# Performance work log

Measured on AMD Instinct MI355X. Metric: run time of the kernel, lower is better.

Reference implementation:

```python
import jax, jax.numpy as jnp
import numpy as np
from jax import lax

B, S, F, D, O = 4096, 256, 32, 64, 16
LABEL = S // 2  # label site index (num_sites // 2)


def setup_inputs() -> dict:
    key = jax.random.key(0)
    k = jax.random.split(key, 6)
    x = jax.random.normal(k[0], (B, S, F), dtype=jnp.float32)
    # Variance-preserving scales so the 256-step chain stays O(1)
    s_edge = 1.0 / np.sqrt(F)
    s_mid = 1.0 / np.sqrt(D * F)
    s_lab = 1.0 / np.sqrt(D * F * D)
    W0 = jax.random.normal(k[1], (F, D), dtype=jnp.float32) * s_edge          # site 0
    W_left = jax.random.normal(k[2], (LABEL - 1, D, F, D), dtype=jnp.float32) * s_mid   # sites 1..LABEL-1
    W_label = jax.random.normal(k[3], (D, F, D, O), dtype=jnp.float32) * s_lab          # site LABEL
    W_right = jax.random.normal(k[4], (S - 2 - LABEL, D, F, D), dtype=jnp.float32) * s_mid  # sites LABEL+1..S-2 (ascending)
    W_last = jax.random.normal(k[5], (D, F), dtype=jnp.float32) * s_edge       # site S-1
    return {"x": x, "W0": W0, "W_left": W_left, "W_label": W_label,
            "W_right": W_right, "W_last": W_last}


def _mps_forward(x, W0, W_left, W_label, W_right, W_last):
    label = W_left.shape[0] + 1
    # left sweep: v_b = x[b,0] @ W0, then v <- v W(x_i)
    v = jnp.einsum('bf,fd->bd', x[:, 0], W0)                 # (B, D)
    xs_left = jnp.moveaxis(x[:, 1:label], 0, 1)              # (L_left, B, F)

    def lstep(v, inp):
        W, xi = inp                                          # (D,F,D), (B,F)
        return jnp.einsum('bd,dfe,bf->be', v, W, xi), None

    v, _ = lax.scan(lstep, v, (W_left, xs_left))

    # right sweep: r_b = W_last @ x[b,-1], then r <- W(x_i) r, i from S-2 down to label+1
    r = jnp.einsum('bf,df->bd', x[:, -1], W_last)            # (B, D)
    xs_right = jnp.moveaxis(x[:, label + 1:-1], 0, 1)        # (L_right, B, F)

    def rstep(r, inp):
        W, xi = inp
        return jnp.einsum('be,dfe,bf->bd', r, W, xi), None

    r, _ = lax.scan(rstep, r, (W_right, xs_right), reverse=True)

    # label site contraction -> logits (B, O)
    return jnp.einsum('bd,dfeo,bf,be->bo', v, W_label, x[:, label], r)


def reference(x, W0, W_left, W_label, W_right, W_last):
    return _mps_forward(x, W0, W_left, W_label, W_right, W_last)
```

## Files before the change

### kernel.cpp

```cpp
#include <hip/hip_runtime.h>


typedef _Float16 half2v __attribute__((ext_vector_type(2)));
typedef _Float16 half8 __attribute__((ext_vector_type(8)));
typedef float f32x16 __attribute__((ext_vector_type(16)));
typedef unsigned int uint4v __attribute__((ext_vector_type(4)));

#define MFMA32(a, b, c) __builtin_amdgcn_mfma_f32_32x32x16_f16((a), (b), (c), 0, 0, 0)

#define VPAD 66

#define WS_WLF 0L
#define WS_WRF 33292288L
#define WS_WLAB 66322432L
#define WS_V 70516736L
#define WS_R 71565312L

__device__ __forceinline__ f32x16 zero16() {
  f32x16 z;
#pragma unroll
  for (int i = 0; i < 16; ++i) z[i] = 0.0f;
  return z;
}

__device__ __forceinline__ unsigned int pack2h(float a, float b) {
  half2v h;
  h[0] = (_Float16)a;
  h[1] = (_Float16)b;
  return __builtin_bit_cast(unsigned int, h);
}

__device__ __forceinline__ half2v splat2(float a) {
  _Float16 x = (_Float16)a;
  half2v h;
  h[0] = x;
  h[1] = x;
  return h;
}

__device__ __forceinline__ half8 mulfrag(const half2v s, const unsigned int* o) {
  uint4v t;
#pragma unroll
  for (int i = 0; i < 4; ++i) {
    half2v b = __builtin_bit_cast(half2v, o[i]);
    half2v p = s * b;
    t[i] = __builtin_bit_cast(unsigned int, p);
  }
  return __builtin_bit_cast(half8, t);
}

__global__ void prep_kernel(const float* __restrict__ wl, const float* __restrict__ wr,
                            const float* __restrict__ wlab,
                            _Float16* __restrict__ wlf, _Float16* __restrict__ wrf,
                            _Float16* __restrict__ wlabf) {
  const long t0 = (long)blockIdx.x * blockDim.x + threadIdx.x;
  const long stride = (long)gridDim.x * blockDim.x;
  const long NL = 127L * 128 * 2 * 64;
  const long NR = 126L * 128 * 2 * 64;
  const long NB = 128L * 32 * 64;

  for (long F = t0; F < NL; F += stride) {
    const int l = (int)(F & 63), t = (int)((F >> 6) & 1);
    const int s = (int)((F >> 7) & 127), site = (int)(F >> 14);
    const int k0 = s * 16 + ((l >> 5) << 3);
    const int d = k0 >> 5, f0 = k0 & 31, e = t * 32 + (l & 31);
    const float* src = wl + (((long)site * 64 + d) * 32 + f0) * 64 + e;
    half8 v;
#pragma unroll
    for (int j = 0; j < 8; ++j) v[j] = (_Float16)src[(long)j * 64];
    *(half8*)(wlf + F * 8) = v;
  }
  for (long F = t0; F < NR; F += stride) {
    const int l = (int)(F & 63), t = (int)((F >> 6) & 1);
    const int s = (int)((F >> 7) & 127), site = (int)(F >> 14);
    const int k0 = s * 16 + ((l >> 5) << 3);
    const int f = k0 >> 6, e0 = k0 & 63, d = t * 32 + (l & 31);
    const float* src = wr + (((long)site * 64 + d) * 32 + f) * 64 + e0;
    half8 v;
#pragma unroll
    for (int j = 0; j < 8; ++j) v[j] = (_Float16)src[j];
    *(half8*)(wrf + F * 8) = v;
  }
  for (long F = t0; F < NB; F += stride) {
    const int l = (int)(F & 63), t = (int)((F >> 6) & 31);
    const int s = (int)(F >> 11);
    const int k0 = s * 16 + ((l >> 5) << 3);
    const int d = k0 >> 5, f0 = k0 & 31;
    const int n = t * 32 + (l & 31);
    const int e = n >> 4, oo = n & 15;
    const float* src = wlab + (((long)d * 32 + f0) * 64 + e) * 16 + oo;
    half8 v;
#pragma unroll
    for (int j = 0; j < 8; ++j) v[j] = (_Float16)src[(long)j * 1024];
    *(half8*)(wlabf + F * 8) = v;
  }
}

__launch_bounds__(1024, 4)
__global__ void chain_kernel(const float* __restrict__ x, const float* __restrict__ w0,
                             const float* __restrict__ wlast,
                             const _Float16* __restrict__ wlf,
                             const _Float16* __restrict__ wrf,
                             float* __restrict__ wsV, float* __restrict__ wsR) {
  __shared__ float vacc[2][32 * VPAD];
  __shared__ unsigned int xsf[2][2][64][4];
  __shared__ unsigned int xplu[2][32][17];
  __shared__ float xinit[32][33];

  const int tid = threadIdx.x;
  const int lane = tid & 63;
  const int wv = tid >> 6;
  const int t = wv & 1;
  const int kq = wv >> 1;
  const int m = lane & 31;
  const int h = lane >> 5;
  const int chain = blockIdx.x >> 7;
  const int b0 = (blockIdx.x & 127) * 32;

  if (tid < 128) {
    const int row = tid >> 2, c8 = (tid & 3) * 8;
    const float* xp = x + ((long)(b0 + row) * 256 + (chain ? 255 : 0)) * 32 + c8;
    const float4 xa = ((const float4*)xp)[0];
    const float4 xb = ((const float4*)xp)[1];
    xinit[row][c8 + 0] = xa.x; xinit[row][c8 + 1] = xa.y;
    xinit[row][c8 + 2] = xa.z; xinit[row][c8 + 3] = xa.w;
    xinit[row][c8 + 4] = xb.x; xinit[row][c8 + 5] = xb.y;
    xinit[row][c8 + 6] = xb.z; xinit[row][c8 + 7] = xb.w;
  }
  __syncthreads();
  {
    const int row = tid >> 5, c = tid & 31;
    float a0 = 0.f, a1 = 0.f;
    if (chain == 0) {
#pragma unroll 8
      for (int f = 0; f < 32; ++f) {
        a0 += xinit[row][f] * w0[f * 64 + c];
        a1 += xinit[row][f] * w0[f * 64 + c + 32];
      }
    } else {
#pragma unroll 8
      for (int f = 0; f < 32; ++f) {
        a0 += xinit[row][f] * wlast[c * 32 + f];
        a1 += xinit[row][f] * wlast[(c + 32) * 32 + f];
      }
    }
    vacc[1][row * VPAD + c] = a0;
    vacc[1][row * VPAD + c + 32] = a1;
  }
  if (tid < 512) {
    const int row = tid >> 4, q = tid & 15;
    const float2 f2 = *(const float2*)(x + ((long)(b0 + row) * 256 + (chain ? 254 : 1)) * 32 + 2 * q);
    const unsigned int pk = pack2h(f2.x, f2.y);
    if (chain == 0)
      xsf[0][q >> 3][((q >> 2) & 1) * 32 + row][q & 3] = pk;
    else
      xplu[0][row][q] = pk;
  }
  __syncthreads();

  const int NIT = chain ? 126 : 127;

  for (int it = 0; it < NIT; ++it) {
    float* P = vacc[it & 1];
    const float* Q = vacc[(it + 1) & 1];
    const int cb = it & 1, nb = (it & 1) ^ 1;

    for (int i = tid; i < 32 * VPAD; i += 1024) P[i] = 0.f;

    half2v vsp[8];
    unsigned int roct[4][4];
    if (chain == 0) {
      const float* src = Q + m * VPAD + kq * 8;
#pragma unroll
      for (int qq = 0; qq < 4; ++qq) {
        const float2 f2 = *(const float2*)(src + 2 * qq);
        vsp[2 * qq] = splat2(f2.x);
        vsp[2 * qq + 1] = splat2(f2.y);
      }
    } else {
      const float* src = Q + m * VPAD + 8 * h;
#pragma unroll
      for (int c = 0; c < 4; ++c)
#pragma unroll
        for (int i = 0; i < 4; ++i) {
          const float2 f2 = *(const float2*)(src + 16 * c + 2 * i);
          roct[c][i] = pack2h(f2.x, f2.y);
        }
    }
    __syncthreads();

    float2 pxf;
    const bool haspx = (it + 1 < NIT) && (tid < 512);
    if (haspx) {
      const int row = tid >> 4, q = tid & 15;
      const int nsite = chain ? (253 - it) : (2 + it);
      pxf = *(const float2*)(x + ((long)(b0 + row) * 256 + nsite) * 32 + 2 * q);
    }

    f32x16 acc = zero16();

    if (chain == 0) {
      unsigned int xo[2][4];
#pragma unroll
      for (int p = 0; p < 2; ++p)
#pragma unroll
        for (int i = 0; i < 4; ++i) xo[p][i] = xsf[cb][p][lane][i];

      const _Float16* wb = wlf + (long)it * 131072 + kq * 16384 + t * 512 + lane * 8;
#pragma unroll
      for (int q = 0; q < 8; ++q) {
        half8 bp0 = *(const half8*)(wb + q * 2048);
        half8 bp1 = *(const half8*)(wb + q * 2048 + 1024);
        half8 a0 = mulfrag(vsp[q], xo[0]);
        half8 a1 = mulfrag(vsp[q], xo[1]);
        acc = MFMA32(a0, bp0, acc);
        acc = MFMA32(a1, bp1, acc);
      }
    } else {
      const _Float16* wb = wrf + (long)(125 - it) * 131072 + kq * 16384 + t * 512 + lane * 8;
#pragma unroll
      for (int q = 0; q < 4; ++q) {
        const int fi = 4 * kq + q;
        const half2v pw = __builtin_bit_cast(half2v, xplu[cb][m][fi >> 1]);
        const _Float16 xv = (fi & 1) ? pw[1] : pw[0];
        half2v sp;
        sp[0] = xv;
        sp[1] = xv;
#pragma unroll
        for (int c = 0; c < 4; ++c) {
          half8 b = *(const half8*)(wb + q * 4096 + c * 1024);
          half8 a = mulfrag(sp, roct[c]);
          acc = MFMA32(a, b, acc);
        }
      }
    }

    if (haspx) {
      const int row = tid >> 4, q = tid & 15;
      const unsigned int pk = pack2h(pxf.x, pxf.y);
      if (chain == 0)
        xsf[nb][q >> 3][((q >> 2) & 1) * 32 + row][q & 3] = pk;
      else
        xplu[nb][row][q] = pk;
    }

#pragma unroll
    for (int gg = 0; gg < 16; ++gg) {
      const int g = (gg + 2 * kq) & 15;
      const int r = (g & 3) + ((g >> 2) << 3) + (h << 2);
      atomicAdd(&P[r * VPAD + t * 32 + m], acc[g]);
    }
    __syncthreads();
  }

  {
    const float* FB = vacc[(NIT - 1) & 1];
    float* dst = (chain ? wsR : wsV) + (long)b0 * 64;
    for (int i = tid; i < 2048; i += 1024) dst[i] = FB[(i >> 6) * VPAD + (i & 63)];
  }
}

__launch_bounds__(1024, 4)
__global__ void label_kernel(const float* __restrict__ x,
                             const _Float16* __restrict__ wlabf,
                             const float* __restrict__ wsV, const float* __restrict__ wsR,
                             float* __restrict__ out) {
  __shared__ float vsh[32 * VPAD];
  __shared__ float rsh[32 * VPAD];
  __shared__ unsigned int xsf[2][64][4];
  __shared__ float lacc[32][17];

  const int tid = threadIdx.x, lane = tid & 63, wv = tid >> 6;
  const int t = wv & 1, kq = wv >> 1;
  const int m = lane & 31, h = lane >> 5;
  const long b0 = (long)blockIdx.x * 32;

  for (int i = tid; i < 2048; i += 1024) {
    vsh[(i >> 6) * VPAD + (i & 63)] = wsV[b0 * 64 + i];
    rsh[(i >> 6) * VPAD + (i & 63)] = wsR[b0 * 64 + i];
  }
  if (tid < 544) ((float*)lacc)[tid] = 0.f;
  if (tid < 512) {
    const int row = tid >> 4, q = tid & 15;
    const float2 f2 = *(const float2*)(x + ((b0 + row) * 256 + 128) * 32 + 2 * q);
    xsf[q >> 3][((q >> 2) & 1) * 32 + row][q & 3] = pack2h(f2.x, f2.y);
  }
  __syncthreads();

  half2v vsp[8];
  {
    const float* src = vsh + m * VPAD + kq * 8;
#pragma unroll
    for (int qq = 0; qq < 4; ++qq) {
      const float2 f2 = *(const float2*)(src + 2 * qq);
      vsp[2 * qq] = splat2(f2.x);
      vsp[2 * qq + 1] = splat2(f2.y);
    }
  }
  unsigned int xo[2][4];
#pragma unroll
  for (int p = 0; p < 2; ++p)
#pragma unroll
    for (int i = 0; i < 4; ++i) xo[p][i] = xsf[p][lane][i];

  float lg[16];
#pragma unroll
  for (int g = 0; g < 16; ++g) lg[g] = 0.f;

  const _Float16* wb = wlabf + (long)kq * 16 * 16384 + t * 512 + lane * 8;
  for (int g2 = 0; g2 < 16; ++g2) {
    f32x16 acc = zero16();
    const _Float16* wg = wb + (long)g2 * 1024;
#pragma unroll
    for (int q = 0; q < 8; ++q) {
      half8 bp0 = *(const half8*)(wg + (long)q * 32768);
      half8 bp1 = *(const half8*)(wg + (long)q * 32768 + 16384);
      half8 a0 = mulfrag(vsp[q], xo[0]);
      half8 a1 = mulfrag(vsp[q], xo[1]);
      acc = MFMA32(a0, bp0, acc);
      acc = MFMA32(a1, bp1, acc);
    }
    const int e = g2 * 4 + t * 2 + (m >> 4);
#pragma unroll
    for (int g = 0; g < 16; ++g) {
      const int r = (g & 3) + ((g >> 2) << 3) + (h << 2);
      lg[g] += acc[g] * rsh[r * VPAD + e];
    }
  }
#pragma unroll
  for (int gg = 0; gg < 16; ++gg) {
    const int g = (gg + 2 * kq) & 15;
    const int r = (g & 3) + ((g >> 2) << 3) + (h << 2);
    atomicAdd(&lacc[r][m & 15], lg[g]);
  }
  __syncthreads();
  if (tid < 512) out[b0 * 16 + tid] = lacc[tid >> 4][tid & 15];
}

extern "C" void kernel_launch(void* const* d_in, const int* in_sizes, int n_in,
                              void* d_out, int out_size, void* d_ws, size_t ws_size,
                              hipStream_t stream) {
  const float* x = (const float*)d_in[0];
  const float* w0 = (const float*)d_in[1];
  const float* wl = (const float*)d_in[2];
  const float* wlab = (const float*)d_in[3];
  const float* wr = (const float*)d_in[4];
  const float* wlast = (const float*)d_in[5];

  char* ws = (char*)d_ws;
  _Float16* wlf = (_Float16*)(ws + WS_WLF);
  _Float16* wrf = (_Float16*)(ws + WS_WRF);
  _Float16* wlabf = (_Float16*)(ws + WS_WLAB);
  float* wsV = (float*)(ws + WS_V);
  float* wsR = (float*)(ws + WS_R);

  prep_kernel<<<2048, 256, 0, stream>>>(wl, wr, wlab, wlf, wrf, wlabf);
  chain_kernel<<<256, 1024, 0, stream>>>(x, w0, wlast, wlf, wrf, wsV, wsR);
  label_kernel<<<128, 1024, 0, stream>>>(x, wlabf, wsV, wsR, (float*)d_out);
}
```

Baseline: 3.598 ms.

## Prefetch weight fragments before barrier and use lgkm-only barriers in chain loop

In the chain kernel, all 16 weight fragments for the step are loaded from global memory into registers at the top of each iteration, before the shared-memory zeroing and the barrier. Their latency can then overlap with the barrier and the LDS reads. __syncthreads is replaced by an s_waitcnt lgkmcnt(0) plus s_barrier, so the barrier does not also wait on outstanding global loads. The x-operand LDS reads are moved ahead of the barrier. The label kernel also batches its weight loads into two groups of eight. This raises register pressure under 1024-thread launch bounds, and the hand-written barrier relies on the global prefetch staying outside the LDS dependency.

```diff
diff --git a/kernel.cpp b/kernel.cpp
--- a/kernel.cpp
+++ b/kernel.cpp
@@ -15,6 +15,12 @@
 #define WS_WLAB 66322432L
 #define WS_V 70516736L
 #define WS_R 71565312L
+
+#define LGKM_BARRIER()                                   \
+  do {                                                   \
+    asm volatile("s_waitcnt lgkmcnt(0)" ::: "memory");   \
+    __builtin_amdgcn_s_barrier();                        \
+  } while (0)
 
 __device__ __forceinline__ f32x16 zero16() {
   f32x16 z;
@@ -165,29 +171,14 @@
     const float* Q = vacc[(it + 1) & 1];
     const int cb = it & 1, nb = (it & 1) ^ 1;
 
-    for (int i = tid; i < 32 * VPAD; i += 1024) P[i] = 0.f;
-
-    half2v vsp[8];
-    unsigned int roct[4][4];
-    if (chain == 0) {
-      const float* src = Q + m * VPAD + kq * 8;
-#pragma unroll
-      for (int qq = 0; qq < 4; ++qq) {
-        const float2 f2 = *(const float2*)(src + 2 * qq);
-        vsp[2 * qq] = splat2(f2.x);
-        vsp[2 * qq + 1] = splat2(f2.y);
-      }
-    } else {
-      const float* src = Q + m * VPAD + 8 * h;
-#pragma unroll
-      for (int c = 0; c < 4; ++c)
-#pragma unroll
-        for (int i = 0; i < 4; ++i) {
-          const float2 f2 = *(const float2*)(src + 16 * c + 2 * i);
-          roct[c][i] = pack2h(f2.x, f2.y);
-        }
-    }
-    __syncthreads();
+    half8 wbuf[16];
+    {
+      const _Float16* wb = (chain == 0)
+          ? (wlf + (long)it * 131072 + kq * 16384 + t * 512 + lane * 8)
+          : (wrf + (long)(125 - it) * 131072 + kq * 16384 + t * 512 + lane * 8);
+#pragma unroll
+      for (int i = 0; i < 16; ++i) wbuf[i] = *(const half8*)(wb + i * 1024);
+    }
 
     float2 pxf;
     const bool haspx = (it + 1 < NIT) && (tid < 512);
@@ -197,40 +188,59 @@
       pxf = *(const float2*)(x + ((long)(b0 + row) * 256 + nsite) * 32 + 2 * q);
     }
 
+    for (int i = tid; i < 32 * VPAD; i += 1024) P[i] = 0.f;
+
+    half2v vsp[8];
+    unsigned int roct[4][4];
+    unsigned int xo[2][4];
+    unsigned int xw0 = 0, xw1 = 0;
+    if (chain == 0) {
+      const float* src = Q + m * VPAD + kq * 8;
+#pragma unroll
+      for (int qq = 0; qq < 4; ++qq) {
+        const float2 f2 = *(const float2*)(src + 2 * qq);
+        vsp[2 * qq] = splat2(f2.x);
+        vsp[2 * qq + 1] = splat2(f2.y);
+      }
+#pragma unroll
+      for (int p = 0; p < 2; ++p)
+#pragma unroll
+        for (int i = 0; i < 4; ++i) xo[p][i] = xsf[cb][p][lane][i];
+    } else {
+      const float* src = Q + m * VPAD + 8 * h;
+#pragma unroll
+      for (int c = 0; c < 4; ++c)
+#pragma unroll
+        for (int i = 0; i < 4; ++i) {
+          const float2 f2 = *(const float2*)(src + 16 * c + 2 * i);
+          roct[c][i] = pack2h(f2.x, f2.y);
+        }
+      xw0 = xplu[cb][m][2 * kq];
+      xw1 = xplu[cb][m][2 * kq + 1];
+    }
+    LGKM_BARRIER();
+
     f32x16 acc = zero16();
-
     if (chain == 0) {
-      unsigned int xo[2][4];
-#pragma unroll
-      for (int p = 0; p < 2; ++p)
-#pragma unroll
-        for (int i = 0; i < 4; ++i) xo[p][i] = xsf[cb][p][lane][i];
-
-      const _Float16* wb = wlf + (long)it * 131072 + kq * 16384 + t * 512 + lane * 8;
 #pragma unroll
       for (int q = 0; q < 8; ++q) {
-        half8 bp0 = *(const half8*)(wb + q * 2048);
-        half8 bp1 = *(const half8*)(wb + q * 2048 + 1024);
         half8 a0 = mulfrag(vsp[q], xo[0]);
+        acc = MFMA32(a0, wbuf[2 * q], acc);
         half8 a1 = mulfrag(vsp[q], xo[1]);
-        acc = MFMA32(a0, bp0, acc);
-        acc = MFMA32(a1, bp1, acc);
+        acc = MFMA32(a1, wbuf[2 * q + 1], acc);
       }
     } else {
-      const _Float16* wb = wrf + (long)(125 - it) * 131072 + kq * 16384 + t * 512 + lane * 8;
 #pragma unroll
       for (int q = 0; q < 4; ++q) {
-        const int fi = 4 * kq + q;
-        const half2v pw = __builtin_bit_cast(half2v, xplu[cb][m][fi >> 1]);
-        const _Float16 xv = (fi & 1) ? pw[1] : pw[0];
+        const half2v pw = __builtin_bit_cast(half2v, (q & 2) ? xw1 : xw0);
+        const _Float16 xv = (q & 1) ? pw[1] : pw[0];
         half2v sp;
         sp[0] = xv;
         sp[1] = xv;
 #pragma unroll
         for (int c = 0; c < 4; ++c) {
-          half8 b = *(const half8*)(wb + q * 4096 + c * 1024);
           half8 a = mulfrag(sp, roct[c]);
-          acc = MFMA32(a, b, acc);
+          acc = MFMA32(a, wbuf[4 * q + c], acc);
         }
       }
     }
@@ -250,7 +260,7 @@
       const int r = (g & 3) + ((g >> 2) << 3) + (h << 2);
       atomicAdd(&P[r * VPAD + t * 32 + m], acc[g]);
     }
-    __syncthreads();
+    LGKM_BARRIER();
   }
 
   {
@@ -311,14 +321,24 @@
   for (int g2 = 0; g2 < 16; ++g2) {
     f32x16 acc = zero16();
     const _Float16* wg = wb + (long)g2 * 1024;
-#pragma unroll
-    for (int q = 0; q < 8; ++q) {
-      half8 bp0 = *(const half8*)(wg + (long)q * 32768);
-      half8 bp1 = *(const half8*)(wg + (long)q * 32768 + 16384);
+    half8 wbuf[8];
+#pragma unroll
+    for (int i = 0; i < 8; ++i) wbuf[i] = *(const half8*)(wg + (long)i * 16384);
+#pragma unroll
+    for (int q = 0; q < 4; ++q) {
       half8 a0 = mulfrag(vsp[q], xo[0]);
+      acc = MFMA32(a0, wbuf[2 * q], acc);
       half8 a1 = mulfrag(vsp[q], xo[1]);
-      acc = MFMA32(a0, bp0, acc);
-      acc = MFMA32(a1, bp1, acc);
+      acc = MFMA32(a1, wbuf[2 * q + 1], acc);
+    }
+#pragma unroll
+    for (int i = 0; i < 8; ++i) wbuf[i] = *(const half8*)(wg + (long)(8 + i) * 16384);
+#pragma unroll
+    for (int q = 4; q < 8; ++q) {
+      half8 a0 = mulfrag(vsp[q], xo[0]);
+      acc = MFMA32(a0, wbuf[2 * (q - 4)], acc);
+      half8 a1 = mulfrag(vsp[q], xo[1]);
+      acc = MFMA32(a1, wbuf[2 * (q - 4) + 1], acc);
     }
     const int e = g2 * 4 + t * 2 + (m >> 4);
 #pragma unroll
```

New measurement: 4.203 ms. 16.8% more time.

## Stream chain weights through LDS ring buffer with async global-to-LDS loads

Applied to the files above, without the earlier changes.

The chain kernel now stages each 32KB weight phase into a 4-slot LDS ring buffer via global_load_lds, issued three phases ahead, with manual vmcnt/barrier waits. The reduction split changes so each wave handles one phase slice from LDS instead of loading directly from global. The label kernel batches its weight loads into register groups of eight before the MFMAs. The aim is to hide global-memory latency in the sequential chain. In exchange it adds 128KB of LDS and a barrier per phase, which lowers occupancy and adds synchronisation.

```diff
diff --git a/kernel.cpp b/kernel.cpp
--- a/kernel.cpp
+++ b/kernel.cpp
@@ -47,6 +47,12 @@
     t[i] = __builtin_bit_cast(unsigned int, p);
   }
   return __builtin_bit_cast(half8, t);
+}
+
+__device__ __forceinline__ void gll16(const _Float16* g, _Float16* l) {
+  __builtin_amdgcn_global_load_lds(
+      (const __attribute__((address_space(1))) void*)g,
+      (__attribute__((address_space(3))) void*)l, 16, 0, 0);
 }
 
 __global__ void prep_kernel(const float* __restrict__ wl, const float* __restrict__ wr,
@@ -102,30 +108,43 @@
                              const _Float16* __restrict__ wlf,
                              const _Float16* __restrict__ wrf,
                              float* __restrict__ wsV, float* __restrict__ wsR) {
+  __shared__ __align__(16) _Float16 wstage[4][16384];
   __shared__ float vacc[2][32 * VPAD];
   __shared__ unsigned int xsf[2][2][64][4];
   __shared__ unsigned int xplu[2][32][17];
-  __shared__ float xinit[32][33];
 
   const int tid = threadIdx.x;
   const int lane = tid & 63;
   const int wv = tid >> 6;
   const int t = wv & 1;
-  const int kq = wv >> 1;
+  const int ks = wv >> 1;
   const int m = lane & 31;
   const int h = lane >> 5;
   const int chain = blockIdx.x >> 7;
   const int b0 = (blockIdx.x & 127) * 32;
-
+  const int NIT = chain ? 126 : 127;
+  const int gmax = NIT * 8 - 1;
+
+  auto stage = [&](int g) {
+    const int gc = (g <= gmax) ? g : gmax;
+    const int st = gc >> 3, ph = gc & 7;
+    const _Float16* base = chain ? (wrf + (long)(125 - st) * 131072)
+                                 : (wlf + (long)st * 131072);
+    const _Float16* gsrc = base + (long)ph * 16384 + (2 * wv) * 512 + lane * 8;
+    _Float16* ldst = &wstage[gc & 3][(2 * wv) * 512];
+    gll16(gsrc, ldst);
+    gll16(gsrc + 512, ldst + 512);
+  };
+
+  float* xinit = (float*)&wstage[0][0];
   if (tid < 128) {
     const int row = tid >> 2, c8 = (tid & 3) * 8;
     const float* xp = x + ((long)(b0 + row) * 256 + (chain ? 255 : 0)) * 32 + c8;
     const float4 xa = ((const float4*)xp)[0];
     const float4 xb = ((const float4*)xp)[1];
-    xinit[row][c8 + 0] = xa.x; xinit[row][c8 + 1] = xa.y;
-    xinit[row][c8 + 2] = xa.z; xinit[row][c8 + 3] = xa.w;
-    xinit[row][c8 + 4] = xb.x; xinit[row][c8 + 5] = xb.y;
-    xinit[row][c8 + 6] = xb.z; xinit[row][c8 + 7] = xb.w;
+    float* d = xinit + row * 33 + c8;
+    d[0] = xa.x; d[1] = xa.y; d[2] = xa.z; d[3] = xa.w;
+    d[4] = xb.x; d[5] = xb.y; d[6] = xb.z; d[7] = xb.w;
   }
   __syncthreads();
   {
@@ -134,14 +153,14 @@
     if (chain == 0) {
 #pragma unroll 8
       for (int f = 0; f < 32; ++f) {
-        a0 += xinit[row][f] * w0[f * 64 + c];
-        a1 += xinit[row][f] * w0[f * 64 + c + 32];
+        a0 += xinit[row * 33 + f] * w0[f * 64 + c];
+        a1 += xinit[row * 33 + f] * w0[f * 64 + c + 32];
       }
     } else {
 #pragma unroll 8
       for (int f = 0; f < 32; ++f) {
-        a0 += xinit[row][f] * wlast[c * 32 + f];
-        a1 += xinit[row][f] * wlast[(c + 32) * 32 + f];
+        a0 += xinit[row * 33 + f] * wlast[c * 32 + f];
+        a1 += xinit[row * 33 + f] * wlast[(c + 32) * 32 + f];
       }
     }
     vacc[1][row * VPAD + c] = a0;
@@ -158,36 +177,15 @@
   }
   __syncthreads();
 
-  const int NIT = chain ? 126 : 127;
+  stage(0);
+  stage(1);
+  stage(2);
 
   for (int it = 0; it < NIT; ++it) {
     float* P = vacc[it & 1];
     const float* Q = vacc[(it + 1) & 1];
-    const int cb = it & 1, nb = (it & 1) ^ 1;
-
-    for (int i = tid; i < 32 * VPAD; i += 1024) P[i] = 0.f;
-
-    half2v vsp[8];
-    unsigned int roct[4][4];
-    if (chain == 0) {
-      const float* src = Q + m * VPAD + kq * 8;
-#pragma unroll
-      for (int qq = 0; qq < 4; ++qq) {
-        const float2 f2 = *(const float2*)(src + 2 * qq);
-        vsp[2 * qq] = splat2(f2.x);
-        vsp[2 * qq + 1] = splat2(f2.y);
-      }
-    } else {
-      const float* src = Q + m * VPAD + 8 * h;
-#pragma unroll
-      for (int c = 0; c < 4; ++c)
-#pragma unroll
-        for (int i = 0; i < 4; ++i) {
-          const float2 f2 = *(const float2*)(src + 16 * c + 2 * i);
-          roct[c][i] = pack2h(f2.x, f2.y);
-        }
-    }
-    __syncthreads();
+    const int cb = it & 1, nb = cb ^ 1;
+    const int it8 = it * 8;
 
     float2 pxf;
     const bool haspx = (it + 1 < NIT) && (tid < 512);
@@ -197,43 +195,62 @@
       pxf = *(const float2*)(x + ((long)(b0 + row) * 256 + nsite) * 32 + 2 * q);
     }
 
-    f32x16 acc = zero16();
-
+    for (int i = tid; i < 32 * VPAD; i += 1024) P[i] = 0.f;
+
+    half2v spl[8];
+    unsigned int oct2[2][4];
     if (chain == 0) {
-      unsigned int xo[2][4];
-#pragma unroll
-      for (int p = 0; p < 2; ++p)
-#pragma unroll
-        for (int i = 0; i < 4; ++i) xo[p][i] = xsf[cb][p][lane][i];
-
-      const _Float16* wb = wlf + (long)it * 131072 + kq * 16384 + t * 512 + lane * 8;
-#pragma unroll
-      for (int q = 0; q < 8; ++q) {
-        half8 bp0 = *(const half8*)(wb + q * 2048);
-        half8 bp1 = *(const half8*)(wb + q * 2048 + 1024);
-        half8 a0 = mulfrag(vsp[q], xo[0]);
-        half8 a1 = mulfrag(vsp[q], xo[1]);
-        acc = MFMA32(a0, bp0, acc);
-        acc = MFMA32(a1, bp1, acc);
+#pragma unroll
+      for (int p = 0; p < 8; ++p) spl[p] = splat2(Q[m * VPAD + 8 * p + ks]);
+#pragma unroll
+      for (int i = 0; i < 4; ++i) {
+        oct2[0][i] = xsf[cb][0][lane][i];
+        oct2[1][i] = xsf[cb][1][lane][i];
       }
     } else {
-      const _Float16* wb = wrf + (long)(125 - it) * 131072 + kq * 16384 + t * 512 + lane * 8;
-#pragma unroll
-      for (int q = 0; q < 4; ++q) {
-        const int fi = 4 * kq + q;
-        const half2v pw = __builtin_bit_cast(half2v, xplu[cb][m][fi >> 1]);
-        const _Float16 xv = (fi & 1) ? pw[1] : pw[0];
-        half2v sp;
-        sp[0] = xv;
-        sp[1] = xv;
-#pragma unroll
-        for (int c = 0; c < 4; ++c) {
-          half8 b = *(const half8*)(wb + q * 4096 + c * 1024);
-          half8 a = mulfrag(sp, roct[c]);
-          acc = MFMA32(a, b, acc);
+      const int kh = ks >> 1;
+#pragma unroll
+      for (int p = 0; p < 8; ++p) {
+        const half2v pw = __builtin_bit_cast(half2v, xplu[cb][m][2 * p + (kh >> 1)]);
+        const _Float16 xv = (kh & 1) ? pw[1] : pw[0];
+        half2v sp; sp[0] = xv; sp[1] = xv;
+        spl[p] = sp;
+      }
+      const int e0 = (ks & 1) * 32 + 8 * h;
+#pragma unroll
+      for (int c = 0; c < 2; ++c)
+#pragma unroll
+        for (int i = 0; i < 4; ++i) {
+          const float2 f2 = *(const float2*)(Q + m * VPAD + e0 + 16 * c + 2 * i);
+          oct2[c][i] = pack2h(f2.x, f2.y);
         }
-      }
-    }
+    }
+    asm volatile("s_waitcnt lgkmcnt(0)" ::: "memory");
+    __builtin_amdgcn_s_barrier();
+    asm volatile("" ::: "memory");
+
+    f32x16 acc = zero16();
+
+#define PHASE(p)                                                               \
+    {                                                                          \
+      asm volatile("s_waitcnt vmcnt(4) lgkmcnt(0)" ::: "memory");              \
+      __builtin_amdgcn_s_barrier();                                            \
+      asm volatile("" ::: "memory");                                           \
+      stage(it8 + (p) + 3);                                                    \
+      {                                                                        \
+        const _Float16* W =                                                    \
+            &wstage[(p) & 3][0] + (4 * ks + t) * 512 + lane * 8;               \
+        const half8 bA = *(const half8*)(W);                                   \
+        const half8 bB = *(const half8*)(W + 1024);                            \
+        const half8 aA = mulfrag(spl[(p)], oct2[0]);                          \
+        const half8 aB = mulfrag(spl[(p)], oct2[1]);                          \
+        acc = MFMA32(aA, bA, acc);                                             \
+        acc = MFMA32(aB, bB, acc);                                             \
+      }                                                                        \
+    }
+
+    PHASE(0) PHASE(1) PHASE(2) PHASE(3) PHASE(4) PHASE(5) PHASE(6) PHASE(7)
+#undef PHASE
 
     if (haspx) {
       const int row = tid >> 4, q = tid & 15;
@@ -246,13 +263,16 @@
 
 #pragma unroll
     for (int gg = 0; gg < 16; ++gg) {
-      const int g = (gg + 2 * kq) & 15;
+      const int g = (gg + 2 * ks) & 15;
       const int r = (g & 3) + ((g >> 2) << 3) + (h << 2);
       atomicAdd(&P[r * VPAD + t * 32 + m], acc[g]);
     }
-    __syncthreads();
-  }
-
+    asm volatile("s_waitcnt lgkmcnt(0)" ::: "memory");
+    __builtin_amdgcn_s_barrier();
+    asm volatile("" ::: "memory");
+  }
+
+  asm volatile("s_waitcnt vmcnt(0)" ::: "memory");
   {
     const float* FB = vacc[(NIT - 1) & 1];
     float* dst = (chain ? wsR : wsV) + (long)b0 * 64;
@@ -311,14 +331,24 @@
   for (int g2 = 0; g2 < 16; ++g2) {
     f32x16 acc = zero16();
     const _Float16* wg = wb + (long)g2 * 1024;
-#pragma unroll
-    for (int q = 0; q < 8; ++q) {
-      half8 bp0 = *(const half8*)(wg + (long)q * 32768);
-      half8 bp1 = *(const half8*)(wg + (long)q * 32768 + 16384);
+    half8 wbuf[8];
+#pragma unroll
+    for (int i = 0; i < 8; ++i) wbuf[i] = *(const half8*)(wg + (long)i * 16384);
+#pragma unroll
+    for (int q = 0; q < 4; ++q) {
       half8 a0 = mulfrag(vsp[q], xo[0]);
+      acc = MFMA32(a0, wbuf[2 * q], acc);
       half8 a1 = mulfrag(vsp[q], xo[1]);
-      acc = MFMA32(a0, bp0, acc);
-      acc = MFMA32(a1, bp1, acc);
+      acc = MFMA32(a1, wbuf[2 * q + 1], acc);
+    }
+#pragma unroll
+    for (int i = 0; i < 8; ++i) wbuf[i] = *(const half8*)(wg + (long)(8 + i) * 16384);
+#pragma unroll
+    for (int q = 4; q < 8; ++q) {
+      half8 a0 = mulfrag(vsp[q], xo[0]);
+      acc = MFMA32(a0, wbuf[2 * (q - 4)], acc);
+      half8 a1 = mulfrag(vsp[q], xo[1]);
+      acc = MFMA32(a1, wbuf[2 * (q - 4) + 1], acc);
     }
     const int e = g2 * 4 + t * 2 + (m >> 4);
 #pragma unroll
```

Measured after the change: 3.459 ms. 1.04x faster.
